# Performance work log

Hardware: AMD Instinct MI355X
Metric: run time of the kernel (lower is better)

Reference implementation:

```python
import math
import numpy as np
import jax, jax.numpy as jnp

C = 8  # hidden multiplicity (num_channels)
B, N = 4, 4096

# ---------- real Wigner 3j (e3nn convention: Frobenius norm 1) ----------

def _su2_cg(l1, l2, l3):
    f = math.factorial
    def cg(m1, m2, m3):
        if m1 + m2 != m3:
            return 0.0
        pref = math.sqrt((2 * l3 + 1) * f(l3 + l1 - l2) * f(l3 - l1 + l2) * f(l1 + l2 - l3) / f(l1 + l2 + l3 + 1))
        pref *= math.sqrt(f(l3 + m3) * f(l3 - m3) * f(l1 - m1) * f(l1 + m1) * f(l2 - m2) * f(l2 + m2))
        s = 0.0
        for k in range(l1 + l2 - l3 + 1):
            d = [k, l1 + l2 - l3 - k, l1 - m1 - k, l2 + m2 - k, l3 - l2 + m1 + k, l3 - l1 - m2 + k]
            if min(d) < 0:
                continue
            s += (-1.0) ** k / np.prod([float(f(x)) for x in d])
        return pref * s
    out = np.zeros((2 * l1 + 1, 2 * l2 + 1, 2 * l3 + 1))
    for i, m1 in enumerate(range(-l1, l1 + 1)):
        for j, m2 in enumerate(range(-l2, l2 + 1)):
            for k, m3 in enumerate(range(-l3, l3 + 1)):
                out[i, j, k] = cg(m1, m2, m3)
    return out

def _q_real_to_complex(l):
    q = np.zeros((2 * l + 1, 2 * l + 1), dtype=np.complex128)
    rs2 = 1.0 / math.sqrt(2.0)
    for m in range(-l, 0):
        q[l + m, l + abs(m)] = rs2
        q[l + m, l - abs(m)] = -1j * rs2
    q[l, l] = 1.0
    for m in range(1, l + 1):
        q[l + m, l + abs(m)] = (-1) ** m * rs2
        q[l + m, l - abs(m)] = 1j * (-1) ** m * rs2
    return (-1j) ** l * q

def _w3j(l1, l2, l3):
    Q1, Q2, Q3 = _q_real_to_complex(l1), _q_real_to_complex(l2), _q_real_to_complex(l3)
    Cc = _su2_cg(l1, l2, l3).astype(np.complex128)
    Cr = np.real(np.einsum('ij,kl,mn,ikm->jln', Q1, Q2, np.conj(Q3), Cc))
    return (Cr / np.linalg.norm(Cr)).astype(np.float32)

# tensor-product paths (selection rules for 4e/6e inputs, 0e/2e SH, 4e/6e outputs)
VAL_PATHS = [(4, 0, 4), (4, 2, 4), (6, 2, 4), (4, 2, 6), (6, 0, 6), (6, 2, 6)]
OUT_PATHS = [(4, 4, 4), (4, 6, 4), (6, 4, 4), (6, 6, 4), (4, 4, 6), (4, 6, 6), (6, 4, 6), (6, 6, 6)]
# path normalization ('element'): fan-in = 3*C for tp_val outputs, 4*C^2 for tp_out outputs
W3J_VAL = [jnp.asarray(_w3j(*p) * math.sqrt((2 * p[2] + 1) / (3.0 * C))) for p in VAL_PATHS]
W3J_OUT = [jnp.asarray(_w3j(*p) * math.sqrt((2 * p[2] + 1) / (4.0 * C * C))) for p in OUT_PATHS]


def _forward(feat, sh_lr, log_s, pos_w, pos_b, w_lin_in, w_val, w_out, w_lin_out):
    b, n, _ = feat.shape
    f4, f6 = feat[..., :9], feat[..., 9:]                      # 1x4e, 1x6e
    f4n = f4 / jnp.maximum(jnp.linalg.norm(f4, axis=-1, keepdims=True), 1e-12)
    f6n = f6 / jnp.maximum(jnp.linalg.norm(f6, axis=-1, keepdims=True), 1e-12)
    s4, s6 = jnp.exp(log_s[0]), jnp.exp(log_s[1])
    scores = s4 * jnp.einsum('bnd,bmd->bnm', f4n, f4n) + s6 * jnp.einsum('bnd,bmd->bnm', f6n, f6n)
    pb = sh_lr @ pos_w + pos_b                                 # (N,)
    scores = scores + (pb[:, None] + pb[None, :])[None]
    attn = jax.nn.softmax(scores.astype(jnp.float32), axis=-1).astype(feat.dtype)

    h4 = f4[:, :, None, :] * w_lin_in[0][None, None, :, None]  # (B,N,C,9)
    h6 = f6[:, :, None, :] * w_lin_in[1][None, None, :, None]  # (B,N,C,13)

    y = {0: sh_lr[:, :1], 2: sh_lr[:, 1:]}                     # (N,1), (N,5)
    hx = {4: h4, 6: h6}
    v = {4: jnp.zeros((b, n, C, 9), feat.dtype), 6: jnp.zeros((b, n, C, 13), feat.dtype)}
    for p, (l1, l2, l3) in enumerate(VAL_PATHS):
        v[l3] = v[l3] + jnp.einsum('bnui,nj,ijk,uw->bnwk', hx[l1], y[l2], W3J_VAL[p], w_val[p])
    vals = jnp.concatenate([v[4].reshape(b, n, 9 * C), v[6].reshape(b, n, 13 * C)], axis=-1)

    ctx = jnp.einsum('bnm,bmd->bnd', attn, vals)               # (B,N,22C)
    cx = {4: ctx[..., :9 * C].reshape(b, n, C, 9), 6: ctx[..., 9 * C:].reshape(b, n, C, 13)}
    o = {4: jnp.zeros((b, n, C, 9), feat.dtype), 6: jnp.zeros((b, n, C, 13), feat.dtype)}
    for p, (l1, l2, l3) in enumerate(OUT_PATHS):
        o[l3] = o[l3] + jnp.einsum('bnui,bnvj,ijk,uvw->bnwk', hx[l1], cx[l2], W3J_OUT[p], w_out[p])

    inv_sc = 1.0 / math.sqrt(C)                                # lin_out fan_in = C
    d4 = jnp.einsum('bnui,u->bni', o[4], w_lin_out[0]) * inv_sc
    d6 = jnp.einsum('bnui,u->bni', o[6], w_lin_out[1]) * inv_sc
    return jnp.concatenate([d4, d6], axis=-1)                  # (B,N,22)


def setup_inputs() -> dict:
    key = jax.random.key(0)
    ks = jax.random.split(key, 8)
    feat = jax.random.normal(ks[0], (B, N, 22), jnp.float32)
    sh_lr = jax.random.normal(ks[1], (N, 6), jnp.float32)
    log_s = jnp.array([math.log(1.0 / 3.0), math.log(1.0 / math.sqrt(13.0))], jnp.float32)
    pos_w = 0.01 * jax.random.normal(ks[2], (6,), jnp.float32)
    pos_b = jnp.zeros((), jnp.float32)
    w_lin_in = jax.random.normal(ks[3], (2, C), jnp.float32)
    w_val = jax.random.normal(ks[4], (6, C, C), jnp.float32)
    w_out = jax.random.normal(ks[5], (8, C, C, C), jnp.float32)
    w_lin_out = jax.random.normal(ks[6], (2, C), jnp.float32)
    return dict(feat=feat, sh_lr=sh_lr, log_s=log_s, pos_w=pos_w, pos_b=pos_b,
                w_lin_in=w_lin_in, w_val=w_val, w_out=w_out, w_lin_out=w_lin_out)


def reference(feat, sh_lr, log_s, pos_w, pos_b, w_lin_in, w_val, w_out, w_lin_out):
    return _forward(feat, sh_lr, log_s, pos_w, pos_b, w_lin_in, w_val, w_out, w_lin_out)
```

## Files before the change

kernel.cpp:

```cpp
#include <hip/hip_runtime.h>
#include <cmath>

#define NN 4096
#define BB 4
#define CCH 8

#define OFF_W3JVAL 0
#define OFF_W3JOUT 2688
#define OFF_CTX0   13568
#define CTXS       1572864
#define OFFB_KGH   25220096ULL
#define OFFB_KGL   26268672ULL
#define OFFB_VG    27317248ULL
#define OFFB_WBH   30462976ULL
#define OFFB_WBL   30493696ULL

typedef short s16x8 __attribute__((ext_vector_type(8)));
typedef _Float16 f16x8 __attribute__((ext_vector_type(8)));
typedef float f32x4 __attribute__((ext_vector_type(4)));
typedef unsigned int u32x4 __attribute__((ext_vector_type(4)));
typedef unsigned int u32x2 __attribute__((ext_vector_type(2)));

static __device__ __forceinline__ unsigned short f2bf(float x){
  unsigned u = __float_as_uint(x);
  return (unsigned short)((u + 0x7FFFu + ((u >> 16) & 1u)) >> 16);
}
static __device__ __forceinline__ float bf2f(unsigned short h){
  return __uint_as_float(((unsigned)h) << 16);
}
static __device__ __forceinline__ unsigned pk2r(float v){
  unsigned short h = f2bf(v);
  unsigned short l = f2bf(v - bf2f(h));
  return ((unsigned)l << 16) | (unsigned)h;
}
static __device__ __forceinline__ unsigned short f2h(float x){
  return __builtin_bit_cast(unsigned short, (_Float16)x);
}
static __device__ __forceinline__ void unpk(u32x4 a, u32x4 b, s16x8& h, s16x8& l){
  u32x4 hw = { __builtin_amdgcn_perm(a[1],a[0],0x05040100u),
               __builtin_amdgcn_perm(a[3],a[2],0x05040100u),
               __builtin_amdgcn_perm(b[1],b[0],0x05040100u),
               __builtin_amdgcn_perm(b[3],b[2],0x05040100u)};
  u32x4 lw = { __builtin_amdgcn_perm(a[1],a[0],0x07060302u),
               __builtin_amdgcn_perm(a[3],a[2],0x07060302u),
               __builtin_amdgcn_perm(b[1],b[0],0x07060302u),
               __builtin_amdgcn_perm(b[3],b[2],0x07060302u)};
  h = __builtin_bit_cast(s16x8, hw);
  l = __builtin_bit_cast(s16x8, lw);
}
static __device__ __forceinline__ void barrier_lds(){
  __asm__ volatile("s_waitcnt lgkmcnt(0)\n\ts_barrier" ::: "memory");
}

static __device__ __forceinline__ void qent(int l, int r, int c, double& re, double& im){
  re=0.0; im=0.0;
  double s = ((l&3)==2)? -1.0 : 1.0;
  const double rs2 = 0.70710678118654752440;
  if(r < l){
    if(c == 2*l - r) re = s*rs2;
    else if(c == r)  im = -s*rs2;
  } else if(r == l){
    if(c == l) re = s;
  } else {
    double sg = ((r-l)&1)? -1.0 : 1.0;
    if(c == r) re = s*sg*rs2;
    else if(c == 2*l - r) im = s*sg*rs2;
  }
}
__global__ __launch_bounds__(256) void k_tab(float* __restrict__ Wv, float* __restrict__ Wo){
  __shared__ double Cc[2197];
  __shared__ double red[256];
  __shared__ double factS[20];
  int t = threadIdx.x;
  int p = blockIdx.x;
  if(t==0){
    double f=1.0; factS[0]=1.0;
    for(int i=1;i<20;i++){ f*=(double)i; factS[i]=f; }
  }
  const int L1[14]={4,4,6,4,6,6, 4,4,6,6,4,4,6,6};
  const int L2[14]={0,2,2,2,0,2, 4,6,4,6,4,6,4,6};
  const int L3[14]={4,4,4,6,6,6, 4,4,4,4,6,6,6,6};
  const int OFF[14]={0,81,486,1071,1656,1825, 0,729,1782,2835,4356,5409,6930,8451};
  int l1=L1[p], l2=L2[p], l3=L3[p];
  int d1=2*l1+1, d2=2*l2+1, d3=2*l3+1;
  int tot = d1*d2*d3;
  float* dst = (p<6) ? (Wv+OFF[p]) : (Wo+OFF[p]);
  double scale = (p<6) ? sqrt((2.0*l3+1.0)/24.0) : sqrt((2.0*l3+1.0)/256.0);
  __syncthreads();
  for(int e=t; e<tot; e+=256){
    int i = e/(d2*d3), rem = e - i*(d2*d3), j = rem/d3, k = rem - j*d3;
    int m1=i-l1, m2=j-l2, m3=k-l3;
    double v=0.0;
    if(m1+m2==m3){
      double pref = sqrt((2.0*l3+1.0)*factS[l3+l1-l2]*factS[l3-l1+l2]*factS[l1+l2-l3]/factS[l1+l2+l3+1]);
      pref *= sqrt(factS[l3+m3]*factS[l3-m3]*factS[l1-m1]*factS[l1+m1]*factS[l2-m2]*factS[l2+m2]);
      double s=0.0;
      for(int kk=0; kk<=l1+l2-l3; kk++){
        int dd0=kk, dd1=l1+l2-l3-kk, dd2=l1-m1-kk, dd3=l2+m2-kk, dd4=l3-l2+m1+kk, dd5=l3-l1-m2+kk;
        int mn=dd0;
        if(dd1<mn)mn=dd1; if(dd2<mn)mn=dd2; if(dd3<mn)mn=dd3; if(dd4<mn)mn=dd4; if(dd5<mn)mn=dd5;
        if(mn<0) continue;
        double prod = factS[dd0]*factS[dd1]*factS[dd2]*factS[dd3]*factS[dd4]*factS[dd5];
        s += ((kk&1)? -1.0:1.0)/prod;
      }
      v = pref*s;
    }
    Cc[e]=v;
  }
  __syncthreads();
  double crloc[9];
  double nacc=0.0;
  #pragma unroll
  for(int itr=0; itr<9; ++itr){
    int e = t + itr*256;
    double re = 0.0;
    if(e < tot){
      int j = e/(d2*d3), rem = e - j*(d2*d3), l = rem/d3, n = rem - l*d3;
      #pragma unroll
      for(int ii=0; ii<2; ii++){
        int i = ii ? (2*l1 - j) : j;
        double q1r,q1i; qent(l1,i,j,q1r,q1i);
        if(ii && i==j){ q1r=0.0; q1i=0.0; }
        #pragma unroll
        for(int kk=0; kk<2; kk++){
          int k = kk ? (2*l2 - l) : l;
          double q2r,q2i; qent(l2,k,l,q2r,q2i);
          if(kk && k==l){ q2r=0.0; q2i=0.0; }
          double ar = q1r*q2r - q1i*q2i;
          double ai = q1r*q2i + q1i*q2r;
          #pragma unroll
          for(int mm=0; mm<2; mm++){
            int m = mm ? (2*l3 - n) : n;
            double q3r,q3i; qent(l3,m,n,q3r,q3i);
            if(mm && m==n){ q3r=0.0; q3i=0.0; }
            double coef = ar*q3r + ai*q3i;
            re += coef * Cc[(i*d2+k)*d3+m];
          }
        }
      }
    }
    crloc[itr]=re;
    nacc += re*re;
  }
  red[t]=nacc;
  __syncthreads();
  #pragma unroll
  for(int s=128;s>0;s>>=1){
    if(t<s) red[t]+=red[t+s];
    __syncthreads();
  }
  double c = scale/sqrt(red[0]);
  #pragma unroll
  for(int itr=0; itr<9; ++itr){
    int e = t + itr*256;
    if(e<tot) dst[e]=(float)(crloc[itr]*c);
  }
}

__global__ void k_weights(const float* __restrict__ wli, const float* __restrict__ wval,
                          const float* __restrict__ wout, const float* __restrict__ wlo,
                          const float* __restrict__ Wv,
                          unsigned short* __restrict__ WBH, unsigned short* __restrict__ WBL){
  __shared__ float bws[48];
  __shared__ float scs[64];
  __shared__ float As[24];
  int t = threadIdx.x;
  if(t<48){
    const int val_l1[6]={0,0,1,0,1,1};
    int p=t>>3, w=t&7;
    float s=0.f;
    for(int u=0;u<8;u++) s = fmaf(wli[val_l1[p]*8+u], wval[(p*8+u)*8+w], s);
    bws[t]=s;
  }
  {
    const int out_l1[8]={0,0,1,1,0,0,1,1};
    const int out_l3[8]={0,0,0,0,1,1,1,1};
    int p=t>>3, v=t&7;
    float s=0.f;
    for(int u=0;u<8;u++){
      float a=wli[out_l1[p]*8+u];
      for(int w=0;w<8;w++) s = fmaf(wout[((p*8+u)*8+v)*8+w]*a, wlo[out_l3[p]*8+w], s);
    }
    scs[t]=s*0.35355339059327373f;
  }
  __syncthreads();
  if(t<24){
    int p=t/3, i3=t-3*p;
    int vp = (p&1)*3 + i3;
    float s=0.f;
    for(int w=0;w<8;w++) s = fmaf(scs[p*8+w], bws[vp*8+w], s);
    As[t]=s;
  }
  __syncthreads();
  int base = blockIdx.x*960;
  for(int k=0;k<15;k++){
    int cell = base + k*64 + t;
    int f = cell/160, c = cell - f*160;
    float v = 0.f;
    if(f < 88 && c < 132){
      int seg = f/22, off = f - seg*22;
      int even = (off < 9);
      int p = 2*seg + (even?0:1);
      int jo = even ? off : off-9;
      int l1, i, jj;
      if(c < 54){ l1=4; i=c/6; jj=c-6*i; }
      else { int cc=c-54; l1=6; i=cc/6; jj=cc-6*i; }
      if(even){
        if(l1==4 && jj==0)      v = As[p*3+0]*Wv[i*9+jo];
        else if(l1==4)          v = As[p*3+1]*Wv[81+(i*5+jj-1)*9+jo];
        else if(jj>=1)          v = As[p*3+2]*Wv[486+(i*5+jj-1)*9+jo];
      } else {
        if(l1==4 && jj>=1)      v = As[p*3+0]*Wv[1071+(i*5+jj-1)*13+jo];
        else if(l1==6 && jj==0) v = As[p*3+1]*Wv[1656+i*13+jo];
        else if(l1==6)          v = As[p*3+2]*Wv[1825+(i*5+jj-1)*13+jo];
      }
    } else if(f==88 && c==132){
      v = 1.0f;
    }
    unsigned short h = f2bf(v);
    WBH[cell] = h;
    WBL[cell] = f2bf(v - bf2f(h));
  }
}

__launch_bounds__(128)
__global__ void k_prep(const float* __restrict__ feat, const float* __restrict__ sh,
                       const float* __restrict__ log_s, const float* __restrict__ pos_w,
                       const float* __restrict__ pos_b,
                       const unsigned short* __restrict__ WBH,
                       const unsigned short* __restrict__ WBL,
                       unsigned short* __restrict__ Kgh, unsigned short* __restrict__ Kgl,
                       unsigned short* __restrict__ Vg){
  __shared__ __align__(16) unsigned int Pbuf[16*164];
  __shared__ unsigned int Po[96*17];
  __shared__ float epbs[16];
  int tid = threadIdx.x;
  int w2 = tid >> 6, lane = tid & 63;
  int lm = lane & 15, quad = lane >> 4;
  int seg = w2*4 + quad;
  int panel = blockIdx.x >> 2, mt = blockIdx.x & 3;
  int idxp = panel*64 + mt*16 + lm;
  int n = idxp & (NN-1);
  const float* fp = feat + (size_t)idxp*22;
  const float* shp = sh + n*6;
  float f[22];
  #pragma unroll
  for(int c=0;c<22;c++) f[c]=fp[c];
  float y[6];
  #pragma unroll
  for(int j=0;j<6;j++) y[j]=shp[j];
  if(tid<16){
    float pb = pos_b[0];
    #pragma unroll
    for(int j=0;j<6;j++) pb = fmaf(y[j], pos_w[j], pb);
    epbs[lm] = __expf(pb);
    float n4=0.f, n6=0.f;
    #pragma unroll
    for(int c=0;c<9;c++) n4 += f[c]*f[c];
    #pragma unroll
    for(int c=9;c<22;c++) n6 += f[c]*f[c];
    n4 = fmaxf(sqrtf(n4), 1e-12f);
    n6 = fmaxf(sqrtf(n6), 1e-12f);
    float s4 = __expf(log_s[0]), s6 = __expf(log_s[1]);
    float a4 = sqrtf(s4)/n4, a6 = sqrtf(s6)/n6;
    unsigned short* kph = Kgh + (size_t)idxp*32;
    unsigned short* kpl = Kgl + (size_t)idxp*32;
    #pragma unroll
    for(int c=0;c<22;c++){
      float qv = f[c] * (c<9 ? a4 : a6);
      unsigned short h = f2bf(qv);
      kph[c]=h; kpl[c]=f2bf(qv - bf2f(h));
    }
    #pragma unroll
    for(int c=22;c<32;c++){ kph[c]=0; kpl[c]=0; }
  }
  #pragma unroll
  for(int j4=0;j4<5;j4++){
    u32x4 wv;
    #pragma unroll
    for(int e=0;e<4;e++){
      int c = seg*20 + j4*4 + e;
      float pv;
      if(c<54){ int i=c/6, jj=c-6*i; pv = f[i]*y[jj]; }
      else if(c<132){ int cc=c-54; int i=cc/6, jj=cc-6*i; pv = f[9+i]*y[jj]; }
      else if(c==132) pv = 1.0f;
      else pv = 0.0f;
      wv[e] = pk2r(pv);
    }
    *(u32x4*)&Pbuf[lm*164 + seg*20 + j4*4] = wv;
  }
  __syncthreads();
  f32x4 acc[3];
  #pragma unroll
  for(int ft=0;ft<3;ft++)
    #pragma unroll
    for(int i=0;i<4;i++) acc[ft][i]=0.f;
  for(int kc=0;kc<5;kc++){
    const u32x4* ap = (const u32x4*)&Pbuf[lm*164 + kc*32 + quad*8];
    s16x8 Ah, Al;
    unpk(ap[0], ap[1], Ah, Al);
    #pragma unroll
    for(int ft=0;ft<3;ft++){
      int ftg = w2*3 + ft;
      size_t bo = (size_t)(ftg*16+lm)*160 + kc*32 + quad*8;
      s16x8 Bh = *(const s16x8*)(WBH + bo);
      s16x8 Bl = *(const s16x8*)(WBL + bo);
      f32x4 a = acc[ft];
      a = __builtin_amdgcn_mfma_f32_16x16x32_bf16(Al, Bl, a, 0,0,0);
      a = __builtin_amdgcn_mfma_f32_16x16x32_bf16(Al, Bh, a, 0,0,0);
      a = __builtin_amdgcn_mfma_f32_16x16x32_bf16(Ah, Bl, a, 0,0,0);
      a = __builtin_amdgcn_mfma_f32_16x16x32_bf16(Ah, Bh, a, 0,0,0);
      acc[ft] = a;
    }
  }
  #pragma unroll
  for(int r=0;r<4;r++){
    float e = epbs[quad*4 + r];
    #pragma unroll
    for(int ft=0;ft<3;ft++){
      int ftg = w2*3 + ft;
      Po[(ftg*16+lm)*17 + quad*4 + r] = (unsigned)f2h(acc[ft][r]*e);
    }
  }
  __syncthreads();
  unsigned int* vO32 = (unsigned int*)(Vg + (size_t)panel*96*64);
  #pragma unroll
  for(int wv=0; wv<6; wv++){
    int idx2 = wv*128 + tid;
    int g = idx2 >> 3, j = idx2 & 7;
    unsigned lo = Po[g*17 + 2*j] & 0xFFFFu;
    unsigned hi = Po[g*17 + 2*j + 1] & 0xFFFFu;
    vO32[g*32 + mt*8 + j] = lo | (hi<<16);
  }
}

#define EST 72
__launch_bounds__(512, 4)
__global__ void k_attn(const unsigned short* __restrict__ Kgh,
                       const unsigned short* __restrict__ Kgl,
                       const unsigned short* __restrict__ Vg,
                       float* __restrict__ ctx0){
  __shared__ __align__(16) unsigned short Es[128*EST];
  int tid = threadIdx.x;
  int lane = tid & 63, w = tid >> 6;
  int lm = lane & 15, quad = lane >> 4;
  int blk = blockIdx.x;
  int b = blk & 3, kh = (blk>>2)&3, qb = blk >> 4;
  int qrow0 = qb * 128;
  const unsigned short* KhB = Kgh + (size_t)b*NN*32;
  const unsigned short* KlB = Kgl + (size_t)b*NN*32;
  const unsigned short* VB  = Vg  + (size_t)b*64*96*64;
  float* ctx = ctx0 + (size_t)kh*CTXS + (size_t)b*NN*96;

  int sq = w & 3;
  int sk = w >> 2;

  s16x8 qh[2], ql[2];
  #pragma unroll
  for(int q2=0;q2<2;q2++){
    size_t ro = (size_t)(qrow0 + (2*sq+q2)*16 + lm)*32 + (size_t)quad*8;
    qh[q2] = *(const s16x8*)(KhB + ro);
    ql[q2] = *(const s16x8*)(KlB + ro);
  }
  f32x4 acc[2][3];
  #pragma unroll
  for(int q2=0;q2<2;q2++)
    #pragma unroll
    for(int ft=0;ft<3;ft++)
      #pragma unroll
      for(int i=0;i<4;i++) acc[q2][ft][i]=0.f;

  #pragma unroll 1
  for(int it=0; it<16; ++it){
    int panel = kh*16 + it;
    int key0 = panel*64;
    s16x8 kfh[2], kfl[2];
    #pragma unroll
    for(int k2=0;k2<2;k2++){
      size_t ko = (size_t)(key0 + (2*sk+k2)*16 + lm)*32 + (size_t)quad*8;
      kfh[k2] = *(const s16x8*)(KhB + ko);
      kfl[k2] = *(const s16x8*)(KlB + ko);
    }
    f16x8 vv[2][3];
    #pragma unroll
    for(int ks=0;ks<2;ks++)
      #pragma unroll
      for(int ft=0;ft<3;ft++){
        size_t vo = (size_t)panel*96*64 + (size_t)((3*sk+ft)*16+lm)*64 + ks*32 + quad*8;
        vv[ks][ft] = *(const f16x8*)(VB + vo);
      }
    unsigned p01[2][2], p23[2][2];
    #pragma unroll
    for(int k2=0;k2<2;k2++)
      #pragma unroll
      for(int q2=0;q2<2;q2++){
        f32x4 s = {0.f,0.f,0.f,0.f};
        s = __builtin_amdgcn_mfma_f32_16x16x32_bf16(kfl[k2], qh[q2], s, 0,0,0);
        s = __builtin_amdgcn_mfma_f32_16x16x32_bf16(kfh[k2], ql[q2], s, 0,0,0);
        s = __builtin_amdgcn_mfma_f32_16x16x32_bf16(kfh[k2], qh[q2], s, 0,0,0);
        p01[k2][q2] = (unsigned)f2h(__expf(s[0])) | ((unsigned)f2h(__expf(s[1]))<<16);
        p23[k2][q2] = (unsigned)f2h(__expf(s[2])) | ((unsigned)f2h(__expf(s[3]))<<16);
      }
    barrier_lds();
    #pragma unroll
    for(int k2=0;k2<2;k2++)
      #pragma unroll
      for(int q2=0;q2<2;q2++){
        int row = (2*sq+q2)*16 + lm;
        int key = (2*sk+k2)*16 + quad*4;
        *(u32x2*)&Es[row*EST + key] = (u32x2){p01[k2][q2], p23[k2][q2]};
      }
    barrier_lds();
    #pragma unroll
    for(int ks=0;ks<2;ks++){
      #pragma unroll
      for(int q2=0;q2<2;q2++){
        f16x8 e = *(const f16x8*)&Es[((2*sq+q2)*16 + lm)*EST + ks*32 + quad*8];
        #pragma unroll
        for(int ft=0;ft<3;ft++)
          acc[q2][ft] = __builtin_amdgcn_mfma_f32_16x16x32_f16(e, vv[ks][ft], acc[q2][ft], 0,0,0);
      }
    }
  }
  #pragma unroll
  for(int q2=0;q2<2;q2++){
    #pragma unroll
    for(int ft=0;ft<3;ft++){
      int col = (3*sk+ft)*16 + lm;
      #pragma unroll
      for(int r=0;r<4;r++){
        int row = qrow0 + (2*sq+q2)*16 + quad*4 + r;
        ctx[(size_t)row*96 + col] = acc[q2][ft][r];
      }
    }
  }
}

__launch_bounds__(256, 2)
__global__ void k_out(const float* __restrict__ feat, const float* __restrict__ ctxA,
                      const float* __restrict__ w3jout, float* __restrict__ out){
  __shared__ float gbuf[64*45];
  __shared__ float fbuf[64*24];
  __shared__ float dls[4*64*13];
  __shared__ float inv[64];
  int tid = threadIdx.x;
  int typ = blockIdx.x & 1;
  int n0 = (blockIdx.x>>1)*64;
  int gc0 = typ*44;
  for(int i=tid;i<64*44;i+=256){
    int pt=i/44, c=i-pt*44;
    const float* base = ctxA + (size_t)(n0+pt)*96 + gc0 + c;
    gbuf[pt*45+c] = base[0]+base[CTXS]+base[2*CTXS]+base[3*CTXS];
  }
  for(int i=tid;i<64*22;i+=256){
    int pt=i/22, c=i-pt*22;
    fbuf[pt*24+c] = feat[(size_t)(n0+pt)*22+c];
  }
  if(tid<64){
    const float* bd = ctxA + (size_t)(n0+tid)*96 + 88;
    inv[tid] = 1.0f/(bd[0]+bd[CTXS]+bd[2*CTXS]+bd[3*CTXS]);
  }
  __syncthreads();
  int lane = tid&63, w = tid>>6;
  float fR[13], gR[13], d[13];
  {
    int FB = (w&2)?9:0;
    int fn = (w&2)?13:9;
    #pragma unroll 13
    for(int i=0;i<13;i++) fR[i] = (i<fn) ? fbuf[lane*24 + FB + i] : 0.f;
    int GBl = (w==0)?0:(w==1)?9:(w==2)?22:31;
    int jn = (w&1)?13:9;
    #pragma unroll 13
    for(int j=0;j<13;j++) gR[j] = (j<jn) ? gbuf[lane*45 + GBl + j] : 0.f;
  }
  #pragma unroll 13
  for(int k=0;k<13;k++) d[k]=0.f;

#define PATHR(ID,JD,KD,WO) \
  _Pragma("unroll") \
  for(int i=0;i<(ID);i++){ float fv=fR[i]; \
    _Pragma("unroll") \
    for(int j=0;j<(JD);j++){ float val=fv*gR[j]; \
      const float* wp = w3jout + (WO) + (i*(JD)+j)*(KD); \
      _Pragma("unroll") \
      for(int k=0;k<(KD);k++) d[k] = fmaf(val, wp[k], d[k]); } }

  int pcase = typ*4 + w;
  switch(pcase){
    case 0: PATHR(9,9,9, 0)       break;
    case 1: PATHR(9,13,9, 729)    break;
    case 2: PATHR(13,9,9, 1782)   break;
    case 3: PATHR(13,13,9, 2835)  break;
    case 4: PATHR(9,9,13, 4356)   break;
    case 5: PATHR(9,13,13, 5409)  break;
    case 6: PATHR(13,9,13, 6930)  break;
    default:PATHR(13,13,13, 8451) break;
  }
#undef PATHR
  {
    float* dp = &dls[(w*64+lane)*13];
    #pragma unroll 13
    for(int k=0;k<13;k++) dp[k]=d[k];
  }
  __syncthreads();
  {
    int KD = typ?13:9;
    int kb = typ?9:0;
    int pt = tid&63, kc = tid>>6;
    float iv = inv[pt];
    #pragma unroll
    for(int e=0;e<4;e++){
      int k = kc*4+e;
      if(k<KD){
        float s = dls[(0*64+pt)*13+k] + dls[(1*64+pt)*13+k]
                + dls[(2*64+pt)*13+k] + dls[(3*64+pt)*13+k];
        out[(size_t)(n0+pt)*22 + kb + k] = s*iv;
      }
    }
  }
}

extern "C" void kernel_launch(void* const* d_in, const int* in_sizes, int n_in,
                              void* d_out, int out_size, void* d_ws, size_t ws_size,
                              hipStream_t stream){
  (void)in_sizes; (void)n_in; (void)out_size; (void)ws_size;
  const float* feat =(const float*)d_in[0];
  const float* sh   =(const float*)d_in[1];
  const float* log_s=(const float*)d_in[2];
  const float* pos_w=(const float*)d_in[3];
  const float* pos_b=(const float*)d_in[4];
  const float* wli  =(const float*)d_in[5];
  const float* wval =(const float*)d_in[6];
  const float* wout =(const float*)d_in[7];
  const float* wlo  =(const float*)d_in[8];
  float* outp=(float*)d_out;
  float* wsf=(float*)d_ws;

  unsigned short* Kgh=(unsigned short*)((char*)d_ws + OFFB_KGH);
  unsigned short* Kgl=(unsigned short*)((char*)d_ws + OFFB_KGL);
  unsigned short* Vg =(unsigned short*)((char*)d_ws + OFFB_VG);
  unsigned short* WBH=(unsigned short*)((char*)d_ws + OFFB_WBH);
  unsigned short* WBL=(unsigned short*)((char*)d_ws + OFFB_WBL);

  hipLaunchKernelGGL(k_tab, dim3(14), dim3(256), 0, stream,
                     wsf+OFF_W3JVAL, wsf+OFF_W3JOUT);
  hipLaunchKernelGGL(k_weights, dim3(16), dim3(64), 0, stream,
                     wli, wval, wout, wlo, wsf+OFF_W3JVAL, WBH, WBL);
  hipLaunchKernelGGL(k_prep, dim3(1024), dim3(128), 0, stream,
                     feat, sh, log_s, pos_w, pos_b, WBH, WBL,
                     Kgh, Kgl, Vg);
  hipLaunchKernelGGL(k_attn, dim3(512), dim3(512), 0, stream,
                     Kgh, Kgl, Vg, wsf+OFF_CTX0);
  hipLaunchKernelGGL(k_out, dim3(512), dim3(256), 0, stream,
                     feat, wsf+OFF_CTX0, wsf+OFF_W3JOUT, outp);
}
```

Measured before the change: 217.0 us.

## Prefetch next K/V panel into registers and double-buffer LDS in attention

```diff
diff --git a/kernel.cpp b/kernel.cpp
--- a/kernel.cpp
+++ b/kernel.cpp
@@ -335,25 +335,25 @@
 }
 
 #define EST 72
-__launch_bounds__(512, 4)
+__launch_bounds__(256, 2)
 __global__ void k_attn(const unsigned short* __restrict__ Kgh,
                        const unsigned short* __restrict__ Kgl,
                        const unsigned short* __restrict__ Vg,
                        float* __restrict__ ctx0){
-  __shared__ __align__(16) unsigned short Es[128*EST];
+  __shared__ __align__(16) unsigned short Es[2][64*EST];
   int tid = threadIdx.x;
   int lane = tid & 63, w = tid >> 6;
   int lm = lane & 15, quad = lane >> 4;
   int blk = blockIdx.x;
   int b = blk & 3, kh = (blk>>2)&3, qb = blk >> 4;
-  int qrow0 = qb * 128;
+  int qrow0 = qb * 64;
   const unsigned short* KhB = Kgh + (size_t)b*NN*32;
   const unsigned short* KlB = Kgl + (size_t)b*NN*32;
   const unsigned short* VB  = Vg  + (size_t)b*64*96*64;
   float* ctx = ctx0 + (size_t)kh*CTXS + (size_t)b*NN*96;
 
-  int sq = w & 3;
-  int sk = w >> 2;
+  int sq = w & 1;
+  int sk = w >> 1;
 
   s16x8 qh[2], ql[2];
   #pragma unroll
@@ -370,55 +370,74 @@
       #pragma unroll
       for(int i=0;i<4;i++) acc[q2][ft][i]=0.f;
 
-  #pragma unroll 1
-  for(int it=0; it<16; ++it){
-    int panel = kh*16 + it;
-    int key0 = panel*64;
-    s16x8 kfh[2], kfl[2];
+  s16x8 kfh[2][2], kfl[2][2];
+  f16x8 vv[2][2][3];
+  {
+    int key0 = (kh*16)*64;
     #pragma unroll
     for(int k2=0;k2<2;k2++){
       size_t ko = (size_t)(key0 + (2*sk+k2)*16 + lm)*32 + (size_t)quad*8;
-      kfh[k2] = *(const s16x8*)(KhB + ko);
-      kfl[k2] = *(const s16x8*)(KlB + ko);
-    }
-    f16x8 vv[2][3];
+      kfh[0][k2] = *(const s16x8*)(KhB + ko);
+      kfl[0][k2] = *(const s16x8*)(KlB + ko);
+    }
     #pragma unroll
     for(int ks=0;ks<2;ks++)
       #pragma unroll
       for(int ft=0;ft<3;ft++){
-        size_t vo = (size_t)panel*96*64 + (size_t)((3*sk+ft)*16+lm)*64 + ks*32 + quad*8;
-        vv[ks][ft] = *(const f16x8*)(VB + vo);
-      }
+        size_t vo = (size_t)(kh*16)*96*64 + (size_t)((3*sk+ft)*16+lm)*64 + ks*32 + quad*8;
+        vv[0][ks][ft] = *(const f16x8*)(VB + vo);
+      }
+  }
+
+  #pragma unroll 2
+  for(int it=0; it<16; ++it){
+    int cur = it&1, nxt = cur^1;
+    int panel = kh*16 + it;
+    if(it<15){
+      int key0n = (panel+1)*64;
+      #pragma unroll
+      for(int k2=0;k2<2;k2++){
+        size_t ko = (size_t)(key0n + (2*sk+k2)*16 + lm)*32 + (size_t)quad*8;
+        kfh[nxt][k2] = *(const s16x8*)(KhB + ko);
+        kfl[nxt][k2] = *(const s16x8*)(KlB + ko);
+      }
+      #pragma unroll
+      for(int ks=0;ks<2;ks++)
+        #pragma unroll
+        for(int ft=0;ft<3;ft++){
+          size_t vo = (size_t)(panel+1)*96*64 + (size_t)((3*sk+ft)*16+lm)*64 + ks*32 + quad*8;
+          vv[nxt][ks][ft] = *(const f16x8*)(VB + vo);
+        }
+    }
     unsigned p01[2][2], p23[2][2];
     #pragma unroll
     for(int k2=0;k2<2;k2++)
       #pragma unroll
       for(int q2=0;q2<2;q2++){
         f32x4 s = {0.f,0.f,0.f,0.f};
-        s = __builtin_amdgcn_mfma_f32_16x16x32_bf16(kfl[k2], qh[q2], s, 0,0,0);
-        s = __builtin_amdgcn_mfma_f32_16x16x32_bf16(kfh[k2], ql[q2], s, 0,0,0);
-        s = __builtin_amdgcn_mfma_f32_16x16x32_bf16(kfh[k2], qh[q2], s, 0,0,0);
+        s = __builtin_amdgcn_mfma_f32_16x16x32_bf16(kfl[cur][k2], qh[q2], s, 0,0,0);
+        s = __builtin_amdgcn_mfma_f32_16x16x32_bf16(kfh[cur][k2], ql[q2], s, 0,0,0);
+        s = __builtin_amdgcn_mfma_f32_16x16x32_bf16(kfh[cur][k2], qh[q2], s, 0,0,0);
         p01[k2][q2] = (unsigned)f2h(__expf(s[0])) | ((unsigned)f2h(__expf(s[1]))<<16);
         p23[k2][q2] = (unsigned)f2h(__expf(s[2])) | ((unsigned)f2h(__expf(s[3]))<<16);
       }
-    barrier_lds();
     #pragma unroll
     for(int k2=0;k2<2;k2++)
       #pragma unroll
       for(int q2=0;q2<2;q2++){
         int row = (2*sq+q2)*16 + lm;
         int key = (2*sk+k2)*16 + quad*4;
-        *(u32x2*)&Es[row*EST + key] = (u32x2){p01[k2][q2], p23[k2][q2]};
+        *(u32x2*)&Es[cur][row*EST + key] = (u32x2){p01[k2][q2], p23[k2][q2]};
       }
     barrier_lds();
     #pragma unroll
     for(int ks=0;ks<2;ks++){
       #pragma unroll
       for(int q2=0;q2<2;q2++){
-        f16x8 e = *(const f16x8*)&Es[((2*sq+q2)*16 + lm)*EST + ks*32 + quad*8];
+        f16x8 e = *(const f16x8*)&Es[cur][((2*sq+q2)*16 + lm)*EST + ks*32 + quad*8];
         #pragma unroll
         for(int ft=0;ft<3;ft++)
-          acc[q2][ft] = __builtin_amdgcn_mfma_f32_16x16x32_f16(e, vv[ks][ft], acc[q2][ft], 0,0,0);
+          acc[q2][ft] = __builtin_amdgcn_mfma_f32_16x16x32_f16(e, vv[cur][ks][ft], acc[q2][ft], 0,0,0);
       }
     }
   }
@@ -549,7 +568,7 @@
   hipLaunchKernelGGL(k_prep, dim3(1024), dim3(128), 0, stream,
                      feat, sh, log_s, pos_w, pos_b, WBH, WBL,
                      Kgh, Kgl, Vg);
-  hipLaunchKernelGGL(k_attn, dim3(512), dim3(512), 0, stream,
+  hipLaunchKernelGGL(k_attn, dim3(1024), dim3(256), 0, stream,
                      Kgh, Kgl, Vg, wsf+OFF_CTX0);
   hipLaunchKernelGGL(k_out, dim3(512), dim3(256), 0, stream,
                      feat, wsf+OFF_CTX0, wsf+OFF_W3JOUT, outp);
```

Result: slower. 303.6 us (+39.9%).
